# Kernel optimization log

Measured on AMD Instinct MI355X. Metric: run time of the kernel, lower is better.

The kernel has to match this reference:

```python
import jax, jax.numpy as jnp
import numpy as np

B, D, H, DEPTH = 1024, 1024, 1024, 4


def setup_inputs() -> dict:
    key = jax.random.key(0)
    k_x, k_w, k_ws, k_bs = jax.random.split(key, 4)
    x = jax.random.normal(k_x, (B, D), dtype=jnp.float32)
    W_enc = jax.random.normal(k_w, (D, H), dtype=jnp.float32) * 0.02
    b_enc = jnp.zeros((H,), dtype=jnp.float32)
    # per-layer CrossNet weights, matching keras random_normal init (stddev=0.05)
    ws = jax.random.normal(k_ws, (DEPTH, H, 1), dtype=jnp.float32) * 0.05
    bs = jax.random.normal(k_bs, (DEPTH, H, 1), dtype=jnp.float32) * 0.05
    return {"x": x, "W_enc": W_enc, "b_enc": b_enc, "ws": ws, "bs": bs}


def reference(x, W_enc, b_enc, ws, bs):
    # encoder Dense
    h = jnp.matmul(x, W_enc) + b_enc  # (B, H)
    x0 = h
    x_l = h
    depth = ws.shape[0]
    for l in range(depth):
        # original: (x0[:, :, None] * x_l[:, None, :]) @ w + b, squeezed.
        # outer[b,i,j] @ w  == x0[b,i] * sum_j x_l[b,j] * w[j]
        s = jnp.matmul(x_l, ws[l])            # (B, 1)
        residual = x0 * s + bs[l][:, 0]       # (B, H)
        x_l = residual + x_l
    return x_l
```

## Files before the change

kernel.cpp:

```cpp
#include <hip/hip_runtime.h>


#define B_SZ 1024
#define D_SZ 1024
#define H_SZ 1024
#define DEPTH 4

typedef _Float16 half4_t __attribute__((ext_vector_type(4)));
typedef _Float16 half8_t __attribute__((ext_vector_type(8)));
typedef float floatx4_t __attribute__((ext_vector_type(4)));

typedef const __attribute__((address_space(1))) unsigned int* gas_ptr;
typedef __attribute__((address_space(3))) unsigned int* las_ptr;

__device__ __forceinline__ void async_copy16(const void* g, void* l) {
    __builtin_amdgcn_global_load_lds((gas_ptr)g, (las_ptr)l, 16, 0, 0);
}

__global__ __launch_bounds__(256) void prep_kernel(
        const float* __restrict__ x, const float* __restrict__ W,
        const float* __restrict__ ws, const float* __restrict__ bs,
        _Float16* __restrict__ xh, _Float16* __restrict__ Wt,
        float* __restrict__ cvec, float* __restrict__ beta4) {
    const int b = blockIdx.x;
    const int t = threadIdx.x;
    if (b < 256) {
        __shared__ float S[64][65];
        const int k0 = (b >> 4) << 6;
        const int n0 = (b & 15) << 6;
#pragma unroll
        for (int i = 0; i < 4; ++i) {
            int idx = (i << 8) + t;
            int r = idx >> 4;
            int c4 = idx & 15;
            float4 v = *(const float4*)(W + (size_t)(k0 + r) * H_SZ + n0 + (c4 << 2));
            S[r][(c4 << 2) + 0] = v.x;
            S[r][(c4 << 2) + 1] = v.y;
            S[r][(c4 << 2) + 2] = v.z;
            S[r][(c4 << 2) + 3] = v.w;
        }
        __syncthreads();
#pragma unroll
        for (int i = 0; i < 4; ++i) {
            int idx = (i << 8) + t;
            int n = idx >> 4;
            int c4 = idx & 15;
            int k = c4 << 2;
            half4_t o;
            o.x = (_Float16)S[k + 0][n];
            o.y = (_Float16)S[k + 1][n];
            o.z = (_Float16)S[k + 2][n];
            o.w = (_Float16)S[k + 3][n];
            *(half4_t*)(Wt + (size_t)(n0 + n) * D_SZ + k0 + k) = o;
        }
    } else if (b < 512) {
        const int base = (b - 256) * 4096;
#pragma unroll
        for (int i = 0; i < 4; ++i) {
            int off = base + (((i << 8) + t) << 2);
            float4 v = *(const float4*)(x + off);
            half4_t o;
            o.x = (_Float16)v.x; o.y = (_Float16)v.y;
            o.z = (_Float16)v.z; o.w = (_Float16)v.w;
            *(half4_t*)(xh + off) = o;
        }
    } else {
        __shared__ float redc[4][3];
        const int j = t << 2;
        float4 b0 = *(const float4*)(bs + 0 * H_SZ + j);
        float4 b1 = *(const float4*)(bs + 1 * H_SZ + j);
        float4 b2 = *(const float4*)(bs + 2 * H_SZ + j);
        float4 b3 = *(const float4*)(bs + 3 * H_SZ + j);
        float4 w1 = *(const float4*)(ws + 1 * H_SZ + j);
        float4 w2 = *(const float4*)(ws + 2 * H_SZ + j);
        float4 w3 = *(const float4*)(ws + 3 * H_SZ + j);
        float4 pre1 = b0;
        float4 pre2 = {pre1.x + b1.x, pre1.y + b1.y, pre1.z + b1.z, pre1.w + b1.w};
        float4 pre3 = {pre2.x + b2.x, pre2.y + b2.y, pre2.z + b2.z, pre2.w + b2.w};
        float4 bt   = {pre3.x + b3.x, pre3.y + b3.y, pre3.z + b3.z, pre3.w + b3.w};
        *(float4*)(beta4 + j) = bt;
        float pp[3];
        pp[0] = pre1.x * w1.x + pre1.y * w1.y + pre1.z * w1.z + pre1.w * w1.w;
        pp[1] = pre2.x * w2.x + pre2.y * w2.y + pre2.z * w2.z + pre2.w * w2.w;
        pp[2] = pre3.x * w3.x + pre3.y * w3.y + pre3.z * w3.z + pre3.w * w3.w;
#pragma unroll
        for (int off = 32; off > 0; off >>= 1) {
#pragma unroll
            for (int l = 0; l < 3; ++l) pp[l] += __shfl_down(pp[l], off, 64);
        }
        if ((t & 63) == 0) {
#pragma unroll
            for (int l = 0; l < 3; ++l) redc[t >> 6][l] = pp[l];
        }
        __syncthreads();
        if (t == 0) {
            cvec[0] = 0.0f;
#pragma unroll
            for (int l = 0; l < 3; ++l)
                cvec[l + 1] = redc[0][l] + redc[1][l] + redc[2][l] + redc[3][l];
        }
    }
}

__global__ __launch_bounds__(512, 2) void gemm_kernel(
        const _Float16* __restrict__ xh, const _Float16* __restrict__ Wt,
        float* __restrict__ h) {
    __shared__ _Float16 As[2][64 * 128];
    __shared__ _Float16 Bs[2][64 * 128];
    const int tid  = threadIdx.x;
    const int lane = tid & 63;
    const int w    = tid >> 6;
    const int m0 = blockIdx.y << 6;
    const int n0 = blockIdx.x << 6;
    const int wm = (w >> 2) << 5;
    const int wn = (w & 3) << 4;

    const int r0 = tid >> 4;
    const int c0 = ((tid & 15) ^ (r0 & 15)) << 3;
    const int r1 = r0 + 32;
    const int c1 = ((tid & 15) ^ (r1 & 15)) << 3;
    const _Float16* aSrc0 = xh + (size_t)(m0 + r0) * D_SZ + c0;
    const _Float16* aSrc1 = xh + (size_t)(m0 + r1) * D_SZ + c1;
    const _Float16* bSrc0 = Wt + (size_t)(n0 + r0) * D_SZ + c0;
    const _Float16* bSrc1 = Wt + (size_t)(n0 + r1) * D_SZ + c1;

    const int ra = wm + (lane & 15);
    const int rb = wn + (lane & 15);
    const int q  = lane >> 4;

    floatx4_t acc0 = {0.0f, 0.0f, 0.0f, 0.0f};
    floatx4_t acc1 = {0.0f, 0.0f, 0.0f, 0.0f};

    async_copy16(aSrc0, &As[0][tid << 3]);
    async_copy16(aSrc1, &As[0][(tid + 512) << 3]);
    async_copy16(bSrc0, &Bs[0][tid << 3]);
    async_copy16(bSrc1, &Bs[0][(tid + 512) << 3]);

    for (int it = 0; it < 8; ++it) {
        __syncthreads();
        if (it + 1 < 8) {
            int k0 = (it + 1) << 7;
            int buf = (it + 1) & 1;
            async_copy16(aSrc0 + k0, &As[buf][tid << 3]);
            async_copy16(aSrc1 + k0, &As[buf][(tid + 512) << 3]);
            async_copy16(bSrc0 + k0, &Bs[buf][tid << 3]);
            async_copy16(bSrc1 + k0, &Bs[buf][(tid + 512) << 3]);
        }
        const _Float16* Ab = As[it & 1];
        const _Float16* Bb = Bs[it & 1];
#pragma unroll
        for (int kk = 0; kk < 4; ++kk) {
            int l = (kk << 2) + q;
            int swz = (l ^ (ra & 15)) << 3;
            half8_t bf = *(const half8_t*)(Bb + rb * 128 + ((l ^ (rb & 15)) << 3));
            half8_t a0 = *(const half8_t*)(Ab + ra * 128 + swz);
            half8_t a1 = *(const half8_t*)(Ab + (ra + 16) * 128 + swz);
            acc0 = __builtin_amdgcn_mfma_f32_16x16x32_f16(a0, bf, acc0, 0, 0, 0);
            acc1 = __builtin_amdgcn_mfma_f32_16x16x32_f16(a1, bf, acc1, 0, 0, 0);
        }
    }

    const int col  = n0 + wn + (lane & 15);
    const int row0 = m0 + wm + (q << 2);
#pragma unroll
    for (int r = 0; r < 4; ++r) {
        h[(size_t)(row0 + r) * H_SZ + col] = acc0[r];
        h[(size_t)(row0 + 16 + r) * H_SZ + col] = acc1[r];
    }
}

__global__ __launch_bounds__(256) void crossnet_kernel(
        float* __restrict__ h, const float* __restrict__ b_enc,
        const float* __restrict__ ws, const float* __restrict__ cvec,
        const float* __restrict__ beta4) {
    const int row = blockIdx.x;
    const int t = threadIdx.x;
    const int j = t << 2;
    float* hr = h + (size_t)row * H_SZ;

    float4 hv = *(const float4*)(hr + j);
    float4 be = *(const float4*)(b_enc + j);
    float x0[4] = {hv.x + be.x, hv.y + be.y, hv.z + be.z, hv.w + be.w};

    float p[DEPTH];
#pragma unroll
    for (int l = 0; l < DEPTH; ++l) {
        float4 wv = *(const float4*)(ws + l * H_SZ + j);
        p[l] = x0[0] * wv.x + x0[1] * wv.y + x0[2] * wv.z + x0[3] * wv.w;
    }
#pragma unroll
    for (int off = 32; off > 0; off >>= 1) {
#pragma unroll
        for (int l = 0; l < DEPTH; ++l) p[l] += __shfl_down(p[l], off, 64);
    }
    __shared__ float red[4][DEPTH];
    if ((t & 63) == 0) {
#pragma unroll
        for (int l = 0; l < DEPTH; ++l) red[t >> 6][l] = p[l];
    }
    __syncthreads();

    float sig = 1.0f;
#pragma unroll
    for (int l = 0; l < DEPTH; ++l) {
        float d = red[0][l] + red[1][l] + red[2][l] + red[3][l];
        float s = sig * d + cvec[l];
        sig += s;
    }
    float4 b4 = *(const float4*)(beta4 + j);
    float4 o = {x0[0] * sig + b4.x, x0[1] * sig + b4.y,
                x0[2] * sig + b4.z, x0[3] * sig + b4.w};
    *(float4*)(hr + j) = o;
}

extern "C" void kernel_launch(void* const* d_in, const int* in_sizes, int n_in,
                              void* d_out, int out_size, void* d_ws, size_t ws_size,
                              hipStream_t stream) {
    const float* x     = (const float*)d_in[0];
    const float* W_enc = (const float*)d_in[1];
    const float* b_enc = (const float*)d_in[2];
    const float* ws    = (const float*)d_in[3];
    const float* bs    = (const float*)d_in[4];
    float* out = (float*)d_out;

    _Float16* xh = (_Float16*)d_ws;
    _Float16* Wt = xh + (size_t)B_SZ * D_SZ;
    float* aux   = (float*)((char*)d_ws + 4u * 1024u * 1024u);
    float* cvec  = aux;
    float* beta4 = aux + 4;

    prep_kernel<<<513, 256, 0, stream>>>(x, W_enc, ws, bs, xh, Wt, cvec, beta4);
    dim3 grid(H_SZ / 64, B_SZ / 64);
    gemm_kernel<<<grid, 512, 0, stream>>>(xh, Wt, out);
    crossnet_kernel<<<B_SZ, 256, 0, stream>>>(out, b_enc, ws, cvec, beta4);
}
```

Before: 80.81 us.

## Fuse CrossNet epilogue into GEMM via last-block-per-row-strip atomic counter

Removes the separate crossnet kernel launch. Each GEMM block adds b_enc on store, then bumps a per-row-strip counter. The last of the 16 column blocks for a 64-row strip runs the CrossNet recurrence over those rows, and the counters are reset in prep_kernel. This saves a launch and the overlap gap, but the tail work is serialized onto 16 blocks of 8 waves each, so the epilogue has limited parallelism.

```diff
diff --git a/kernel.cpp b/kernel.cpp
--- a/kernel.cpp
+++ b/kernel.cpp
@@ -21,7 +21,8 @@
         const float* __restrict__ x, const float* __restrict__ W,
         const float* __restrict__ ws, const float* __restrict__ bs,
         _Float16* __restrict__ xh, _Float16* __restrict__ Wt,
-        float* __restrict__ cvec, float* __restrict__ beta4) {
+        float* __restrict__ cvec, float* __restrict__ beta4,
+        int* __restrict__ cnt) {
     const int b = blockIdx.x;
     const int t = threadIdx.x;
     if (b < 256) {
@@ -65,6 +66,7 @@
             *(half4_t*)(xh + off) = o;
         }
     } else {
+        if (t < 16) cnt[t] = 0;
         __shared__ float redc[4][3];
         const int j = t << 2;
         float4 b0 = *(const float4*)(bs + 0 * H_SZ + j);
@@ -102,11 +104,14 @@
     }
 }
 
-__global__ __launch_bounds__(512, 2) void gemm_kernel(
+__global__ __launch_bounds__(512, 2) void gemm_cross_kernel(
         const _Float16* __restrict__ xh, const _Float16* __restrict__ Wt,
-        float* __restrict__ h) {
+        const float* __restrict__ b_enc, const float* __restrict__ ws,
+        const float* __restrict__ cvec, const float* __restrict__ beta4,
+        float* __restrict__ h, int* __restrict__ cnt) {
     __shared__ _Float16 As[2][64 * 128];
     __shared__ _Float16 Bs[2][64 * 128];
+    __shared__ int lastFlag;
     const int tid  = threadIdx.x;
     const int lane = tid & 63;
     const int w    = tid >> 6;
@@ -162,55 +167,64 @@
 
     const int col  = n0 + wn + (lane & 15);
     const int row0 = m0 + wm + (q << 2);
+    const float be = b_enc[col];
 #pragma unroll
     for (int r = 0; r < 4; ++r) {
-        h[(size_t)(row0 + r) * H_SZ + col] = acc0[r];
-        h[(size_t)(row0 + 16 + r) * H_SZ + col] = acc1[r];
-    }
-}
-
-__global__ __launch_bounds__(256) void crossnet_kernel(
-        float* __restrict__ h, const float* __restrict__ b_enc,
-        const float* __restrict__ ws, const float* __restrict__ cvec,
-        const float* __restrict__ beta4) {
-    const int row = blockIdx.x;
-    const int t = threadIdx.x;
-    const int j = t << 2;
-    float* hr = h + (size_t)row * H_SZ;
-
-    float4 hv = *(const float4*)(hr + j);
-    float4 be = *(const float4*)(b_enc + j);
-    float x0[4] = {hv.x + be.x, hv.y + be.y, hv.z + be.z, hv.w + be.w};
-
-    float p[DEPTH];
-#pragma unroll
-    for (int l = 0; l < DEPTH; ++l) {
-        float4 wv = *(const float4*)(ws + l * H_SZ + j);
-        p[l] = x0[0] * wv.x + x0[1] * wv.y + x0[2] * wv.z + x0[3] * wv.w;
-    }
-#pragma unroll
-    for (int off = 32; off > 0; off >>= 1) {
-#pragma unroll
-        for (int l = 0; l < DEPTH; ++l) p[l] += __shfl_down(p[l], off, 64);
-    }
-    __shared__ float red[4][DEPTH];
-    if ((t & 63) == 0) {
-#pragma unroll
-        for (int l = 0; l < DEPTH; ++l) red[t >> 6][l] = p[l];
-    }
+        h[(size_t)(row0 + r) * H_SZ + col] = acc0[r] + be;
+        h[(size_t)(row0 + 16 + r) * H_SZ + col] = acc1[r] + be;
+    }
+
+    __threadfence();
     __syncthreads();
-
-    float sig = 1.0f;
-#pragma unroll
-    for (int l = 0; l < DEPTH; ++l) {
-        float d = red[0][l] + red[1][l] + red[2][l] + red[3][l];
-        float s = sig * d + cvec[l];
-        sig += s;
-    }
-    float4 b4 = *(const float4*)(beta4 + j);
-    float4 o = {x0[0] * sig + b4.x, x0[1] * sig + b4.y,
-                x0[2] * sig + b4.z, x0[3] * sig + b4.w};
-    *(float4*)(hr + j) = o;
+    if (tid == 0) lastFlag = (atomicAdd(&cnt[blockIdx.y], 1) == 15);
+    __syncthreads();
+    if (!lastFlag) return;
+    __threadfence();
+
+    const int lc = lane << 2;
+    float4 wv[DEPTH][4];
+    float4 bt[4];
+#pragma unroll
+    for (int l = 0; l < DEPTH; ++l)
+#pragma unroll
+        for (int i = 0; i < 4; ++i)
+            wv[l][i] = *(const float4*)(ws + l * H_SZ + (i << 8) + lc);
+#pragma unroll
+    for (int i = 0; i < 4; ++i)
+        bt[i] = *(const float4*)(beta4 + (i << 8) + lc);
+    const float4 cv = *(const float4*)cvec;
+    const float cvl[4] = {cv.x, cv.y, cv.z, cv.w};
+
+    for (int rr = 0; rr < 8; ++rr) {
+        float* hr = h + (size_t)(m0 + (w << 3) + rr) * H_SZ;
+        float4 xv[4];
+#pragma unroll
+        for (int i = 0; i < 4; ++i) xv[i] = *(const float4*)(hr + (i << 8) + lc);
+        float p[DEPTH] = {0.f, 0.f, 0.f, 0.f};
+#pragma unroll
+        for (int l = 0; l < DEPTH; ++l)
+#pragma unroll
+            for (int i = 0; i < 4; ++i)
+                p[l] += xv[i].x * wv[l][i].x + xv[i].y * wv[l][i].y +
+                        xv[i].z * wv[l][i].z + xv[i].w * wv[l][i].w;
+#pragma unroll
+        for (int off = 32; off > 0; off >>= 1) {
+#pragma unroll
+            for (int l = 0; l < DEPTH; ++l) p[l] += __shfl_xor(p[l], off, 64);
+        }
+        float sig = 1.0f;
+#pragma unroll
+        for (int l = 0; l < DEPTH; ++l) {
+            float s = sig * p[l] + cvl[l];
+            sig += s;
+        }
+#pragma unroll
+        for (int i = 0; i < 4; ++i) {
+            float4 o = {xv[i].x * sig + bt[i].x, xv[i].y * sig + bt[i].y,
+                        xv[i].z * sig + bt[i].z, xv[i].w * sig + bt[i].w};
+            *(float4*)(hr + (i << 8) + lc) = o;
+        }
+    }
 }
 
 extern "C" void kernel_launch(void* const* d_in, const int* in_sizes, int n_in,
@@ -228,9 +242,10 @@
     float* aux   = (float*)((char*)d_ws + 4u * 1024u * 1024u);
     float* cvec  = aux;
     float* beta4 = aux + 4;
-
-    prep_kernel<<<513, 256, 0, stream>>>(x, W_enc, ws, bs, xh, Wt, cvec, beta4);
+    int*   cnt   = (int*)(aux + 4 + H_SZ);
+
+    prep_kernel<<<513, 256, 0, stream>>>(x, W_enc, ws, bs, xh, Wt, cvec, beta4, cnt);
     dim3 grid(H_SZ / 64, B_SZ / 64);
-    gemm_kernel<<<grid, 512, 0, stream>>>(xh, Wt, out);
-    crossnet_kernel<<<B_SZ, 256, 0, stream>>>(out, b_enc, ws, cvec, beta4);
-}
+    gemm_cross_kernel<<<grid, 512, 0, stream>>>(xh, Wt, b_enc, ws, cvec, beta4,
+                                                out, cnt);
+}
```

Measured after the change: 149.5 us. 85.0% more time.
